# Performance work log

Measured on AMD Instinct MI355X. Metric: run time of the kernel, lower is better.

## Reference

```python
import jax, jax.numpy as jnp
import numpy as np

B, T, E, H = 2, 2048, 1024, 16
S = E // H
LN_EPS = 1e-5


def _layer_norm(x, w, b):
    # normalize over last axis (head dim s)
    mu = jnp.mean(x, axis=-1, keepdims=True)
    var = jnp.mean(jnp.square(x - mu), axis=-1, keepdims=True)
    return (x - mu) * jax.lax.rsqrt(var + LN_EPS) * w + b


def setup_inputs() -> dict:
    key = jax.random.key(0)
    ks = jax.random.split(key, 7)
    scale = 0.02
    return {
        "queries": jax.random.normal(ks[0], (B, T, E), dtype=jnp.float32),
        "keys": jax.random.normal(ks[1], (B, T, E), dtype=jnp.float32),
        "values": jax.random.normal(ks[2], (B, T, E), dtype=jnp.float32),
        "Wq": jax.random.normal(ks[3], (E, E), dtype=jnp.float32) * scale,
        "Wk": jax.random.normal(ks[4], (E, E), dtype=jnp.float32) * scale,
        "Wv": jax.random.normal(ks[5], (E, E), dtype=jnp.float32) * scale,
        "Wo": jax.random.normal(ks[6], (E, E), dtype=jnp.float32) * scale,
        "bo": jnp.zeros((E,), dtype=jnp.float32),
        "q_ln_w": jnp.ones((S,), dtype=jnp.float32),
        "q_ln_b": jnp.zeros((S,), dtype=jnp.float32),
        "k_ln_w": jnp.ones((S,), dtype=jnp.float32),
        "k_ln_b": jnp.zeros((S,), dtype=jnp.float32),
    }


def reference(queries, keys, values, Wq, Wk, Wv, Wo, bo, q_ln_w, q_ln_b, k_ln_w, k_ln_b):
    b, tq, e = queries.shape
    tk = keys.shape[1]
    h, s = H, S

    q = (queries @ Wq).reshape(b, tq, h, s)
    k = (keys @ Wk).reshape(b, tk, h, s)
    v = (values @ Wv).reshape(b, tk, h, s)

    # kqnorm: per-head LayerNorm over s
    q = _layer_norm(q, q_ln_w, q_ln_b)
    k = _layer_norm(k, k_ln_w, k_ln_b)

    # NOTE: original scales q and k each by emb**(-1/4) (NOT head_dim)
    inv4 = jnp.asarray(e, q.dtype) ** -0.25
    q = q * inv4
    k = k * inv4

    dot = jnp.einsum("bqhs,bkhs->bhqk", q, k)  # [b,h,tq,tk]

    # causal mask (mask_diagonal=False -> keep diagonal): mask j > i
    causal = jnp.tril(jnp.ones((tq, tk), dtype=bool))
    dot = jnp.where(causal, dot, jnp.asarray(-jnp.inf, dot.dtype))

    attn = jax.nn.softmax(dot, axis=-1)

    out = jnp.einsum("bhqk,bkhs->bqhs", attn, v).reshape(b, tq, e)
    return out @ Wo + bo
```

## Files before the change

### kernel.cpp

```cpp
#include <hip/hip_runtime.h>

#define Tdim 2048
#define Edim 1024
#define Hdim 16
#define Sdim 64
#define Mdim 4096
#define LN_EPS 1e-5f
#define QKSCALE 0.21233045007200477f

typedef __bf16 bf16x8 __attribute__((ext_vector_type(8)));
typedef float f32x4 __attribute__((ext_vector_type(4)));

__device__ __forceinline__ unsigned short f2bf(float f) {
  union { float f; unsigned int u; } c; c.f = f;
  unsigned int u = c.u;
  return (unsigned short)((u + 0x7FFFu + ((u >> 16) & 1u)) >> 16);
}

__device__ __forceinline__ float exp2fast(float x) {
  float r;
  asm("v_exp_f32 %0, %1" : "=v"(r) : "v"(x));
  return r;
}

__device__ __forceinline__ void gl_lds16(const void* g, void* l) {
  __builtin_amdgcn_global_load_lds(
      (const __attribute__((address_space(1))) void*)g,
      (__attribute__((address_space(3))) void*)l, 16, 0, 0);
}

__device__ __forceinline__ unsigned int pk2bf(unsigned int lo, unsigned int hi) {
  return __builtin_amdgcn_perm(hi, lo, 0x07060302u);
}

__global__ __launch_bounds__(256) void cvt_k(
    const float* __restrict__ X0, const float* __restrict__ X1, const float* __restrict__ X2,
    unsigned short* __restrict__ Y0, unsigned short* __restrict__ Y1,
    unsigned short* __restrict__ Y2) {
  const float* X = blockIdx.z == 0 ? X0 : blockIdx.z == 1 ? X1 : X2;
  unsigned short* Y = blockIdx.z == 0 ? Y0 : blockIdx.z == 1 ? Y1 : Y2;
  size_t i = ((size_t)blockIdx.x * 256 + threadIdx.x) * 8;
  uint4 a = *(const uint4*)&X[i];
  uint4 b = *(const uint4*)&X[i + 4];
  uint4 o;
  o.x = pk2bf(a.x, a.y);
  o.y = pk2bf(a.z, a.w);
  o.z = pk2bf(b.x, b.y);
  o.w = pk2bf(b.z, b.w);
  *(uint4*)&Y[i] = o;
}

__global__ __launch_bounds__(256) void wconv_k(
    const float* __restrict__ W0, const float* __restrict__ W1,
    const float* __restrict__ W2, const float* __restrict__ W3,
    unsigned short* __restrict__ O0, unsigned short* __restrict__ O1,
    unsigned short* __restrict__ O2, unsigned short* __restrict__ O3) {
  const float* W = blockIdx.z == 0 ? W0 : blockIdx.z == 1 ? W1 : blockIdx.z == 2 ? W2 : W3;
  unsigned short* O = blockIdx.z == 0 ? O0 : blockIdx.z == 1 ? O1 : blockIdx.z == 2 ? O2 : O3;
  __shared__ float tile[32][33];
  int n0 = blockIdx.x * 32, k0 = blockIdx.y * 32;
  int tx = threadIdx.x, ty = threadIdx.y;
  for (int yy = ty; yy < 32; yy += 8)
    tile[yy][tx] = W[(size_t)(k0 + yy) * Edim + n0 + tx];
  __syncthreads();
  for (int yy = ty; yy < 32; yy += 8)
    O[(size_t)(n0 + yy) * Edim + k0 + tx] = f2bf(tile[tx][yy]);
}

__global__ __launch_bounds__(256) void qkv_k(
    const unsigned short* __restrict__ Qa, const unsigned short* __restrict__ Ka,
    const unsigned short* __restrict__ Va,
    const unsigned short* __restrict__ Bq, const unsigned short* __restrict__ Bk,
    const unsigned short* __restrict__ Bv,
    const float* __restrict__ qlnw, const float* __restrict__ qlnb,
    const float* __restrict__ klnw, const float* __restrict__ klnb,
    unsigned short* __restrict__ Oq, unsigned short* __restrict__ Ok,
    unsigned short* __restrict__ Ov) {
  __shared__ unsigned short As[2][128 * 64];
  __shared__ unsigned short Bs[2][128 * 64];
  const int z = blockIdx.z;
  const unsigned short* A = z == 0 ? Qa : z == 1 ? Ka : Va;
  const unsigned short* Bt = z == 0 ? Bq : z == 1 ? Bk : Bv;
  const float* lnw = z == 0 ? qlnw : klnw;
  const float* lnb = z == 0 ? qlnb : klnb;
  unsigned short* obf = z == 0 ? Oq : z == 1 ? Ok : Ov;
  const bool doLN = z < 2;

  int tid = threadIdx.x, lane = tid & 63, w = tid >> 6;
  int wr = w >> 1, wc = w & 1;
  int lg = lane >> 4, l15 = lane & 15;
  int lr = lane >> 3, ls = lane & 7;
  int m0 = blockIdx.y * 128, n0 = blockIdx.x * 128;

  f32x4 acc[4][4];
#pragma unroll
  for (int i = 0; i < 4; ++i)
#pragma unroll
    for (int j = 0; j < 4; ++j) acc[i][j] = f32x4{0.f, 0.f, 0.f, 0.f};

  auto stage = [&](int buf, int ks) {
    int k0 = ks * 64;
#pragma unroll
    for (int q = 0; q < 4; ++q) {
      int c = w * 4 + q, r = c * 8 + lr;
      gl_lds16(&A[(size_t)(m0 + r) * Edim + k0 + ((ls ^ (r & 7)) * 8)], &As[buf][c * 512]);
    }
#pragma unroll
    for (int q = 0; q < 4; ++q) {
      int c = w * 4 + q, r = c * 8 + lr;
      gl_lds16(&Bt[(size_t)(n0 + r) * Edim + k0 + ((ls ^ (r & 7)) * 8)], &Bs[buf][c * 512]);
    }
  };

  stage(0, 0);
  for (int ks = 0; ks < 16; ++ks) {
    int cur = ks & 1;
    __syncthreads();
    if (ks + 1 < 16) stage(cur ^ 1, ks + 1);
    __builtin_amdgcn_s_setprio(1);
#pragma unroll
    for (int kx = 0; kx < 2; ++kx) {
      bf16x8 a[4], bb[4];
#pragma unroll
      for (int i = 0; i < 4; ++i) {
        int r = wr * 64 + i * 16 + l15;
        a[i] = *(const bf16x8*)&As[cur][r * 64 + (((kx * 4 + lg) ^ (r & 7)) * 8)];
      }
#pragma unroll
      for (int j = 0; j < 4; ++j) {
        int r = wc * 64 + j * 16 + l15;
        bb[j] = *(const bf16x8*)&Bs[cur][r * 64 + (((kx * 4 + lg) ^ (r & 7)) * 8)];
      }
#pragma unroll
      for (int i = 0; i < 4; ++i)
#pragma unroll
        for (int j = 0; j < 4; ++j)
          acc[i][j] = __builtin_amdgcn_mfma_f32_16x16x32_bf16(a[i], bb[j], acc[i][j], 0, 0, 0);
    }
    __builtin_amdgcn_s_setprio(0);
  }

  int mb = m0 + wr * 64;
  int h = (n0 >> 6) + wc;
#pragma unroll
  for (int i = 0; i < 4; ++i) {
#pragma unroll
    for (int r = 0; r < 4; ++r) {
      float xv[4];
#pragma unroll
      for (int j = 0; j < 4; ++j) xv[j] = acc[i][j][r];
      float outv[4];
      if (doLN) {
        float sum = xv[0] + xv[1] + xv[2] + xv[3];
        float sq = xv[0] * xv[0] + xv[1] * xv[1] + xv[2] * xv[2] + xv[3] * xv[3];
#pragma unroll
        for (int off = 1; off < 16; off <<= 1) {
          sum += __shfl_xor(sum, off);
          sq += __shfl_xor(sq, off);
        }
        float mean = sum * (1.f / 64.f);
        float var = sq * (1.f / 64.f) - mean * mean;
        float rstd = rsqrtf(var + LN_EPS);
#pragma unroll
        for (int j = 0; j < 4; ++j) {
          int s = j * 16 + l15;
          outv[j] = ((xv[j] - mean) * rstd * lnw[s] + lnb[s]) * QKSCALE;
        }
      } else {
#pragma unroll
        for (int j = 0; j < 4; ++j) outv[j] = xv[j];
      }
      int m = mb + i * 16 + (lg << 2) + r;
      int bb2 = m >> 11, tt = m & 2047;
      size_t base = ((size_t)(bb2 * Hdim + h) * Tdim + tt) * Sdim;
#pragma unroll
      for (int j = 0; j < 4; ++j) obf[base + j * 16 + l15] = f2bf(outv[j]);
    }
  }
}

__global__ __launch_bounds__(256) void gemmo_k(
    const unsigned short* __restrict__ A, const unsigned short* __restrict__ Bt,
    const float* __restrict__ bias, float* __restrict__ ofp) {
  __shared__ unsigned short As[2][128 * 64];
  __shared__ unsigned short Bs[2][64 * 64];
  int tid = threadIdx.x, lane = tid & 63, w = tid >> 6;
  int wr = w >> 1, wc = w & 1;
  int lg = lane >> 4, l15 = lane & 15;
  int lr = lane >> 3, ls = lane & 7;
  int m0 = blockIdx.y * 128, n0 = blockIdx.x * 64;

  f32x4 acc[4][2];
#pragma unroll
  for (int i = 0; i < 4; ++i)
#pragma unroll
    for (int j = 0; j < 2; ++j) acc[i][j] = f32x4{0.f, 0.f, 0.f, 0.f};

  auto stage = [&](int buf, int ks) {
    int k0 = ks * 64;
#pragma unroll
    for (int q = 0; q < 4; ++q) {
      int c = w * 4 + q, r = c * 8 + lr;
      gl_lds16(&A[(size_t)(m0 + r) * Edim + k0 + ((ls ^ (r & 7)) * 8)], &As[buf][c * 512]);
    }
#pragma unroll
    for (int q = 0; q < 2; ++q) {
      int c = w * 2 + q, r = c * 8 + lr;
      gl_lds16(&Bt[(size_t)(n0 + r) * Edim + k0 + ((ls ^ (r & 7)) * 8)], &Bs[buf][c * 512]);
    }
  };

  stage(0, 0);
  for (int ks = 0; ks < 16; ++ks) {
    int cur = ks & 1;
    __syncthreads();
    if (ks + 1 < 16) stage(cur ^ 1, ks + 1);
    __builtin_amdgcn_s_setprio(1);
#pragma unroll
    for (int kx = 0; kx < 2; ++kx) {
      bf16x8 a[4], bb[2];
#pragma unroll
      for (int i = 0; i < 4; ++i) {
        int r = wr * 64 + i * 16 + l15;
        a[i] = *(const bf16x8*)&As[cur][r * 64 + (((kx * 4 + lg) ^ (r & 7)) * 8)];
      }
#pragma unroll
      for (int j = 0; j < 2; ++j) {
        int r = wc * 32 + j * 16 + l15;
        bb[j] = *(const bf16x8*)&Bs[cur][r * 64 + (((kx * 4 + lg) ^ (r & 7)) * 8)];
      }
#pragma unroll
      for (int i = 0; i < 4; ++i)
#pragma unroll
        for (int j = 0; j < 2; ++j)
          acc[i][j] = __builtin_amdgcn_mfma_f32_16x16x32_bf16(a[i], bb[j], acc[i][j], 0, 0, 0);
    }
    __builtin_amdgcn_s_setprio(0);
  }

  int mb = m0 + wr * 64, nb = n0 + wc * 32;
#pragma unroll
  for (int i = 0; i < 4; ++i)
#pragma unroll
    for (int r = 0; r < 4; ++r) {
      int m = mb + i * 16 + (lg << 2) + r;
#pragma unroll
      for (int j = 0; j < 2; ++j) {
        int n = nb + j * 16 + l15;
        ofp[(size_t)m * Edim + n] = acc[i][j][r] + bias[n];
      }
    }
}

__global__ __launch_bounds__(256) void flash_k(
    const unsigned short* __restrict__ Qn, const unsigned short* __restrict__ Kn,
    const unsigned short* __restrict__ Vb, unsigned short* __restrict__ Ob) {
  __shared__ unsigned short Qs[64 * 64];
  __shared__ unsigned short Ks[2][64 * 64];
  __shared__ unsigned short Vt[2][64 * 64];
  __shared__ unsigned short Ps[4][16 * 64];

  int wid0 = blockIdx.y * gridDim.x + blockIdx.x;
  int wid = (wid0 & 7) * 64 + (wid0 >> 3);
  int x = wid & 15, bh = wid >> 4;

  int tid = threadIdx.x, lane = tid & 63, w = tid >> 6;
  int lg = lane >> 4, l15 = lane & 15;
  int lr = lane >> 3, ls = lane & 7;
  int vl = tid >> 4, vs0 = (tid & 15) * 4;
  const unsigned short* Kg = Kn + (size_t)bh * Tdim * Sdim;
  const unsigned short* Vg = Vb + (size_t)bh * Tdim * Sdim;
  int b = bh >> 4, h = bh & 15;

  uint2 vreg[4];
  auto ldV = [&](int t) {
    const unsigned short* p = Vg + (size_t)t * 64 * 64;
#pragma unroll
    for (int j = 0; j < 4; ++j) vreg[j] = *(const uint2*)&p[(j * 16 + vl) * 64 + vs0];
  };
  auto stV = [&](unsigned short* dst) {
#pragma unroll
    for (int st = 0; st < 4; ++st) {
      int s = vs0 + st;
      unsigned int e[4];
#pragma unroll
      for (int j = 0; j < 4; ++j) {
        unsigned int wrd = (st & 2) ? vreg[j].y : vreg[j].x;
        e[j] = (st & 1) ? (wrd >> 16) : (wrd & 0xffffu);
      }
      uint2 wv;
      wv.x = e[0] | (e[1] << 16);
      wv.y = e[2] | (e[3] << 16);
      *(uint2*)((char*)dst + s * 128 + (((vl >> 1) ^ (s & 7)) * 16) + (vl & 1) * 8) = wv;
    }
  };

  for (int ph = 0; ph < 2; ++ph) {
    int qseg = ph ? (31 - x) : x;
    const unsigned short* Qg = Qn + ((size_t)bh * Tdim + (size_t)qseg * 64) * Sdim;
    int nt = qseg + 1;

#pragma unroll
    for (int q = 0; q < 2; ++q) {
      int c = w * 2 + q, r = c * 8 + lr;
      gl_lds16(&Qg[(size_t)r * 64 + ((ls ^ (r & 7)) * 8)], &Qs[c * 512]);
      gl_lds16(&Kg[(size_t)r * 64 + ((ls ^ (r & 7)) * 8)], &Ks[0][c * 512]);
    }
    ldV(0);
    stV(&Vt[0][0]);

    f32x4 sf[4], o[4];
    float mrun[4], lrun[4];
#pragma unroll
    for (int r = 0; r < 4; ++r) {
      mrun[r] = -1e30f;
      lrun[r] = 0.f;
      o[r] = f32x4{0.f, 0.f, 0.f, 0.f};
    }
    __syncthreads();

    for (int t = 0; t < nt; ++t) {
      int cur = t & 1;
      if (t + 1 < nt) {
#pragma unroll
        for (int q = 0; q < 2; ++q) {
          int c = w * 2 + q, r = c * 8 + lr;
          gl_lds16(&Kg[((size_t)(t + 1) * 64 + r) * 64 + ((ls ^ (r & 7)) * 8)],
                   &Ks[cur ^ 1][c * 512]);
        }
        ldV(t + 1);
      }
#pragma unroll
      for (int j = 0; j < 4; ++j) sf[j] = f32x4{0.f, 0.f, 0.f, 0.f};
      __builtin_amdgcn_s_setprio(1);
#pragma unroll
      for (int kx = 0; kx < 2; ++kx) {
        int rq = w * 16 + l15;
        bf16x8 aq = *(const bf16x8*)&Qs[rq * 64 + (((kx * 4 + lg) ^ (rq & 7)) * 8)];
#pragma unroll
        for (int j = 0; j < 4; ++j) {
          int rk = j * 16 + l15;
          bf16x8 bk = *(const bf16x8*)&Ks[cur][rk * 64 + (((kx * 4 + lg) ^ (rk & 7)) * 8)];
          sf[j] = __builtin_amdgcn_mfma_f32_16x16x32_bf16(aq, bk, sf[j], 0, 0, 0);
        }
      }
      __builtin_amdgcn_s_setprio(0);
      if (t == qseg) {
#pragma unroll
        for (int j = 0; j < 4; ++j)
#pragma unroll
          for (int rr = 0; rr < 4; ++rr)
            if (j * 16 + l15 > w * 16 + (lg << 2) + rr) sf[j][rr] = -1e30f;
      }
      float mx[4];
#pragma unroll
      for (int rr = 0; rr < 4; ++rr) {
        float m0v = fmaxf(fmaxf(sf[0][rr], sf[1][rr]), fmaxf(sf[2][rr], sf[3][rr]));
#pragma unroll
        for (int off = 1; off < 16; off <<= 1) m0v = fmaxf(m0v, __shfl_xor(m0v, off));
        mx[rr] = m0v;
      }
      int fastok = (mx[0] <= mrun[0] + 8.f) && (mx[1] <= mrun[1] + 8.f) &&
                   (mx[2] <= mrun[2] + 8.f) && (mx[3] <= mrun[3] + 8.f);
      if (!__all(fastok)) {
#pragma unroll
        for (int rr = 0; rr < 4; ++rr) {
          float mnew = fmaxf(mrun[rr], mx[rr]);
          float alpha = exp2fast(mrun[rr] - mnew);
          mrun[rr] = mnew;
          lrun[rr] *= alpha;
#pragma unroll
          for (int js = 0; js < 4; ++js) o[js][rr] *= alpha;
        }
      }
#pragma unroll
      for (int rr = 0; rr < 4; ++rr) {
        float p0 = exp2fast(sf[0][rr] - mrun[rr]);
        float p1 = exp2fast(sf[1][rr] - mrun[rr]);
        float p2 = exp2fast(sf[2][rr] - mrun[rr]);
        float p3 = exp2fast(sf[3][rr] - mrun[rr]);
        lrun[rr] += (p0 + p1) + (p2 + p3);
        union { float f; unsigned int u; } c0{p0}, c1{p1}, c2{p2}, c3{p3};
        uint2 wv;
        wv.x = pk2bf(c0.u, c1.u);
        wv.y = pk2bf(c2.u, c3.u);
        int qr = (lg << 2) + rr;
        *(uint2*)((char*)&Ps[w][0] + qr * 128 + (((l15 >> 1) ^ (qr & 7)) * 16) +
                  (l15 & 1) * 8) = wv;
      }
      __builtin_amdgcn_s_setprio(1);
#pragma unroll
      for (int kx = 0; kx < 2; ++kx) {
        bf16x8 ap = *(const bf16x8*)((char*)&Ps[w][0] + l15 * 128 +
                                     (((kx * 4 + lg) ^ (l15 & 7)) * 16));
#pragma unroll
        for (int js = 0; js < 4; ++js) {
          int rv = js * 16 + l15;
          bf16x8 bv = *(const bf16x8*)((char*)&Vt[cur][0] + rv * 128 +
                                       (((kx * 4 + lg) ^ (rv & 7)) * 16));
          o[js] = __builtin_amdgcn_mfma_f32_16x16x32_bf16(ap, bv, o[js], 0, 0, 0);
        }
      }
      __builtin_amdgcn_s_setprio(0);
      if (t + 1 < nt) stV(&Vt[cur ^ 1][0]);
      __syncthreads();
    }

#pragma unroll
    for (int rr = 0; rr < 4; ++rr) {
      float l = lrun[rr];
#pragma unroll
      for (int off = 1; off < 16; off <<= 1) l += __shfl_xor(l, off);
      float inv = 1.f / l;
      int tg = qseg * 64 + w * 16 + (lg << 2) + rr;
      size_t base = ((size_t)b * Tdim + tg) * Edim + h * 64;
#pragma unroll
      for (int js = 0; js < 4; ++js) Ob[base + js * 16 + l15] = f2bf(o[js][rr] * inv);
    }
  }
}

extern "C" void kernel_launch(void* const* d_in, const int* in_sizes, int n_in,
                              void* d_out, int out_size, void* d_ws, size_t ws_size,
                              hipStream_t stream) {
  const float* queries = (const float*)d_in[0];
  const float* keys    = (const float*)d_in[1];
  const float* values  = (const float*)d_in[2];
  const float* Wq = (const float*)d_in[3];
  const float* Wk = (const float*)d_in[4];
  const float* Wv = (const float*)d_in[5];
  const float* Wo = (const float*)d_in[6];
  const float* bo = (const float*)d_in[7];
  const float* qlnw = (const float*)d_in[8];
  const float* qlnb = (const float*)d_in[9];
  const float* klnw = (const float*)d_in[10];
  const float* klnb = (const float*)d_in[11];
  float* out = (float*)d_out;

  unsigned short* Wtq = (unsigned short*)d_ws;
  unsigned short* Wtk = Wtq + 1024 * 1024;
  unsigned short* Wtv = Wtk + 1024 * 1024;
  unsigned short* Wto = Wtv + 1024 * 1024;
  unsigned short* Qn  = Wto + 1024 * 1024;
  unsigned short* Kn  = Qn + (size_t)Mdim * Edim;
  unsigned short* Vb  = Kn + (size_t)Mdim * Edim;
  unsigned short* Qa  = Vb + (size_t)Mdim * Edim;
  unsigned short* Ka  = Qa + (size_t)Mdim * Edim;
  unsigned short* Va  = Ka + (size_t)Mdim * Edim;
  unsigned short* Ob  = Qa;

  cvt_k<<<dim3(2048, 1, 3), 256, 0, stream>>>(queries, keys, values, Qa, Ka, Va);
  wconv_k<<<dim3(32, 32, 4), dim3(32, 8), 0, stream>>>(Wq, Wk, Wv, Wo, Wtq, Wtk, Wtv, Wto);
  qkv_k<<<dim3(8, 32, 3), 256, 0, stream>>>(Qa, Ka, Va, Wtq, Wtk, Wtv,
                                            qlnw, qlnb, klnw, klnb, Qn, Kn, Vb);
  flash_k<<<dim3(16, 32), 256, 0, stream>>>(Qn, Kn, Vb, Ob);
  gemmo_k<<<dim3(16, 32), 256, 0, stream>>>(Ob, Wto, bo, out);
}
```

Baseline: 247.2 us.

## Pre-transpose V in projection, pipeline QK ahead of softmax, remap blocks

The QKV projection now writes V transposed as [b,h,s,t] by swapping operand roles for z==2, so the flash kernel can load V tiles straight into LDS with async global-to-LDS copies. This replaces the register load and in-LDS transpose. The flash kernel triple-buffers K and computes the next tile's QK^T before the current tile's softmax and PV, to overlap MFMA with exp work. It also keeps a single running max per wave instead of per row, and truncates P to bf16 instead of rounding. Both GEMMs use 1D grids with an XCD-aware block remap to improve L2 locality. The shared per-wave max and the truncation may cost some accuracy, and the transposed V stores are strided.

After: 275.5 us. +11.4%, slower.

```diff
diff --git a/kernel.cpp b/kernel.cpp
--- a/kernel.cpp
+++ b/kernel.cpp
@@ -78,19 +78,20 @@
     unsigned short* __restrict__ Ov) {
   __shared__ unsigned short As[2][128 * 64];
   __shared__ unsigned short Bs[2][128 * 64];
-  const int z = blockIdx.z;
+  int f = blockIdx.x;
+  int L = (f & 7) * 96 + (f >> 3);
+  int bx = L & 7, by = (L >> 3) & 31, z = L >> 8;
   const unsigned short* A = z == 0 ? Qa : z == 1 ? Ka : Va;
   const unsigned short* Bt = z == 0 ? Bq : z == 1 ? Bk : Bv;
   const float* lnw = z == 0 ? qlnw : klnw;
   const float* lnb = z == 0 ? qlnb : klnb;
   unsigned short* obf = z == 0 ? Oq : z == 1 ? Ok : Ov;
-  const bool doLN = z < 2;
 
   int tid = threadIdx.x, lane = tid & 63, w = tid >> 6;
   int wr = w >> 1, wc = w & 1;
   int lg = lane >> 4, l15 = lane & 15;
   int lr = lane >> 3, ls = lane & 7;
-  int m0 = blockIdx.y * 128, n0 = blockIdx.x * 128;
+  int m0 = by * 128, n0 = bx * 128;
 
   f32x4 acc[4][4];
 #pragma unroll
@@ -108,6 +109,118 @@
 #pragma unroll
     for (int q = 0; q < 4; ++q) {
       int c = w * 4 + q, r = c * 8 + lr;
+      gl_lds16(&Bt[(size_t)(n0 + r) * Edim + k0 + ((ls ^ (r & 7)) * 8)], &Bs[buf][c * 512]);
+    }
+  };
+
+  stage(0, 0);
+  for (int ks = 0; ks < 16; ++ks) {
+    int cur = ks & 1;
+    __syncthreads();
+    if (ks + 1 < 16) stage(cur ^ 1, ks + 1);
+    const unsigned short* pA = (z == 2) ? &Bs[cur][0] : &As[cur][0];
+    const unsigned short* pB = (z == 2) ? &As[cur][0] : &Bs[cur][0];
+    __builtin_amdgcn_s_setprio(1);
+#pragma unroll
+    for (int kx = 0; kx < 2; ++kx) {
+      bf16x8 a[4], bb[4];
+#pragma unroll
+      for (int i = 0; i < 4; ++i) {
+        int r = wr * 64 + i * 16 + l15;
+        a[i] = *(const bf16x8*)&pA[r * 64 + (((kx * 4 + lg) ^ (r & 7)) * 8)];
+      }
+#pragma unroll
+      for (int j = 0; j < 4; ++j) {
+        int r = wc * 64 + j * 16 + l15;
+        bb[j] = *(const bf16x8*)&pB[r * 64 + (((kx * 4 + lg) ^ (r & 7)) * 8)];
+      }
+#pragma unroll
+      for (int i = 0; i < 4; ++i)
+#pragma unroll
+        for (int j = 0; j < 4; ++j)
+          acc[i][j] = __builtin_amdgcn_mfma_f32_16x16x32_bf16(a[i], bb[j], acc[i][j], 0, 0, 0);
+    }
+    __builtin_amdgcn_s_setprio(0);
+  }
+
+  if (z < 2) {
+    int mb = m0 + wr * 64;
+    int h = (n0 >> 6) + wc;
+#pragma unroll
+    for (int i = 0; i < 4; ++i) {
+#pragma unroll
+      for (int r = 0; r < 4; ++r) {
+        float xv[4];
+#pragma unroll
+        for (int j = 0; j < 4; ++j) xv[j] = acc[i][j][r];
+        float sum = xv[0] + xv[1] + xv[2] + xv[3];
+        float sq = xv[0] * xv[0] + xv[1] * xv[1] + xv[2] * xv[2] + xv[3] * xv[3];
+#pragma unroll
+        for (int off = 1; off < 16; off <<= 1) {
+          sum += __shfl_xor(sum, off);
+          sq += __shfl_xor(sq, off);
+        }
+        float mean = sum * (1.f / 64.f);
+        float var = sq * (1.f / 64.f) - mean * mean;
+        float rstd = rsqrtf(var + LN_EPS);
+        int m = mb + i * 16 + (lg << 2) + r;
+        int bb2 = m >> 11, tt = m & 2047;
+        size_t base = ((size_t)(bb2 * Hdim + h) * Tdim + tt) * Sdim;
+#pragma unroll
+        for (int j = 0; j < 4; ++j) {
+          int s = j * 16 + l15;
+          float ov = ((xv[j] - mean) * rstd * lnw[s] + lnb[s]) * QKSCALE;
+          obf[base + s] = f2bf(ov);
+        }
+      }
+    }
+  } else {
+#pragma unroll
+    for (int i = 0; i < 4; ++i)
+#pragma unroll
+      for (int r = 0; r < 4; ++r) {
+        int hc = n0 + wr * 64 + i * 16 + (lg << 2) + r;
+        int h = hc >> 6, s = hc & 63;
+#pragma unroll
+        for (int j = 0; j < 4; ++j) {
+          int tk = m0 + wc * 64 + j * 16 + l15;
+          int bb2 = tk >> 11, tt = tk & 2047;
+          obf[(((size_t)(bb2 * Hdim + h) * Sdim + s)) * Tdim + tt] = f2bf(acc[i][j][r]);
+        }
+      }
+  }
+}
+
+__global__ __launch_bounds__(256) void gemmo_k(
+    const unsigned short* __restrict__ A, const unsigned short* __restrict__ Bt,
+    const float* __restrict__ bias, float* __restrict__ ofp) {
+  __shared__ unsigned short As[2][128 * 64];
+  __shared__ unsigned short Bs[2][64 * 64];
+  int f = blockIdx.x;
+  int L = (f & 7) * 64 + (f >> 3);
+  int bx = L & 15, by = L >> 4;
+  int tid = threadIdx.x, lane = tid & 63, w = tid >> 6;
+  int wr = w >> 1, wc = w & 1;
+  int lg = lane >> 4, l15 = lane & 15;
+  int lr = lane >> 3, ls = lane & 7;
+  int m0 = by * 128, n0 = bx * 64;
+
+  f32x4 acc[4][2];
+#pragma unroll
+  for (int i = 0; i < 4; ++i)
+#pragma unroll
+    for (int j = 0; j < 2; ++j) acc[i][j] = f32x4{0.f, 0.f, 0.f, 0.f};
+
+  auto stage = [&](int buf, int ks) {
+    int k0 = ks * 64;
+#pragma unroll
+    for (int q = 0; q < 4; ++q) {
+      int c = w * 4 + q, r = c * 8 + lr;
+      gl_lds16(&A[(size_t)(m0 + r) * Edim + k0 + ((ls ^ (r & 7)) * 8)], &As[buf][c * 512]);
+    }
+#pragma unroll
+    for (int q = 0; q < 2; ++q) {
+      int c = w * 2 + q, r = c * 8 + lr;
       gl_lds16(&Bt[(size_t)(n0 + r) * Edim + k0 + ((ls ^ (r & 7)) * 8)], &Bs[buf][c * 512]);
     }
   };
@@ -120,111 +233,13 @@
     __builtin_amdgcn_s_setprio(1);
 #pragma unroll
     for (int kx = 0; kx < 2; ++kx) {
-      bf16x8 a[4], bb[4];
+      bf16x8 a[4], bb[2];
 #pragma unroll
       for (int i = 0; i < 4; ++i) {
         int r = wr * 64 + i * 16 + l15;
         a[i] = *(const bf16x8*)&As[cur][r * 64 + (((kx * 4 + lg) ^ (r & 7)) * 8)];
       }
 #pragma unroll
-      for (int j = 0; j < 4; ++j) {
-        int r = wc * 64 + j * 16 + l15;
-        bb[j] = *(const bf16x8*)&Bs[cur][r * 64 + (((kx * 4 + lg) ^ (r & 7)) * 8)];
-      }
-#pragma unroll
-      for (int i = 0; i < 4; ++i)
-#pragma unroll
-        for (int j = 0; j < 4; ++j)
-          acc[i][j] = __builtin_amdgcn_mfma_f32_16x16x32_bf16(a[i], bb[j], acc[i][j], 0, 0, 0);
-    }
-    __builtin_amdgcn_s_setprio(0);
-  }
-
-  int mb = m0 + wr * 64;
-  int h = (n0 >> 6) + wc;
-#pragma unroll
-  for (int i = 0; i < 4; ++i) {
-#pragma unroll
-    for (int r = 0; r < 4; ++r) {
-      float xv[4];
-#pragma unroll
-      for (int j = 0; j < 4; ++j) xv[j] = acc[i][j][r];
-      float outv[4];
-      if (doLN) {
-        float sum = xv[0] + xv[1] + xv[2] + xv[3];
-        float sq = xv[0] * xv[0] + xv[1] * xv[1] + xv[2] * xv[2] + xv[3] * xv[3];
-#pragma unroll
-        for (int off = 1; off < 16; off <<= 1) {
-          sum += __shfl_xor(sum, off);
-          sq += __shfl_xor(sq, off);
-        }
-        float mean = sum * (1.f / 64.f);
-        float var = sq * (1.f / 64.f) - mean * mean;
-        float rstd = rsqrtf(var + LN_EPS);
-#pragma unroll
-        for (int j = 0; j < 4; ++j) {
-          int s = j * 16 + l15;
-          outv[j] = ((xv[j] - mean) * rstd * lnw[s] + lnb[s]) * QKSCALE;
-        }
-      } else {
-#pragma unroll
-        for (int j = 0; j < 4; ++j) outv[j] = xv[j];
-      }
-      int m = mb + i * 16 + (lg << 2) + r;
-      int bb2 = m >> 11, tt = m & 2047;
-      size_t base = ((size_t)(bb2 * Hdim + h) * Tdim + tt) * Sdim;
-#pragma unroll
-      for (int j = 0; j < 4; ++j) obf[base + j * 16 + l15] = f2bf(outv[j]);
-    }
-  }
-}
-
-__global__ __launch_bounds__(256) void gemmo_k(
-    const unsigned short* __restrict__ A, const unsigned short* __restrict__ Bt,
-    const float* __restrict__ bias, float* __restrict__ ofp) {
-  __shared__ unsigned short As[2][128 * 64];
-  __shared__ unsigned short Bs[2][64 * 64];
-  int tid = threadIdx.x, lane = tid & 63, w = tid >> 6;
-  int wr = w >> 1, wc = w & 1;
-  int lg = lane >> 4, l15 = lane & 15;
-  int lr = lane >> 3, ls = lane & 7;
-  int m0 = blockIdx.y * 128, n0 = blockIdx.x * 64;
-
-  f32x4 acc[4][2];
-#pragma unroll
-  for (int i = 0; i < 4; ++i)
-#pragma unroll
-    for (int j = 0; j < 2; ++j) acc[i][j] = f32x4{0.f, 0.f, 0.f, 0.f};
-
-  auto stage = [&](int buf, int ks) {
-    int k0 = ks * 64;
-#pragma unroll
-    for (int q = 0; q < 4; ++q) {
-      int c = w * 4 + q, r = c * 8 + lr;
-      gl_lds16(&A[(size_t)(m0 + r) * Edim + k0 + ((ls ^ (r & 7)) * 8)], &As[buf][c * 512]);
-    }
-#pragma unroll
-    for (int q = 0; q < 2; ++q) {
-      int c = w * 2 + q, r = c * 8 + lr;
-      gl_lds16(&Bt[(size_t)(n0 + r) * Edim + k0 + ((ls ^ (r & 7)) * 8)], &Bs[buf][c * 512]);
-    }
-  };
-
-  stage(0, 0);
-  for (int ks = 0; ks < 16; ++ks) {
-    int cur = ks & 1;
-    __syncthreads();
-    if (ks + 1 < 16) stage(cur ^ 1, ks + 1);
-    __builtin_amdgcn_s_setprio(1);
-#pragma unroll
-    for (int kx = 0; kx < 2; ++kx) {
-      bf16x8 a[4], bb[2];
-#pragma unroll
-      for (int i = 0; i < 4; ++i) {
-        int r = wr * 64 + i * 16 + l15;
-        a[i] = *(const bf16x8*)&As[cur][r * 64 + (((kx * 4 + lg) ^ (r & 7)) * 8)];
-      }
-#pragma unroll
       for (int j = 0; j < 2; ++j) {
         int r = wc * 32 + j * 16 + l15;
         bb[j] = *(const bf16x8*)&Bs[cur][r * 64 + (((kx * 4 + lg) ^ (r & 7)) * 8)];
@@ -255,10 +270,10 @@
 __global__ __launch_bounds__(256) void flash_k(
     const unsigned short* __restrict__ Qn, const unsigned short* __restrict__ Kn,
     const unsigned short* __restrict__ Vb, unsigned short* __restrict__ Ob) {
-  __shared__ unsigned short Qs[64 * 64];
-  __shared__ unsigned short Ks[2][64 * 64];
-  __shared__ unsigned short Vt[2][64 * 64];
-  __shared__ unsigned short Ps[4][16 * 64];
+  __shared__ unsigned short Qs[4096];
+  __shared__ unsigned short Ks[3][4096];
+  __shared__ unsigned short Vt[2][4096];
+  __shared__ unsigned short Ps[4][1024];
 
   int wid0 = blockIdx.y * gridDim.x + blockIdx.x;
   int wid = (wid0 & 7) * 64 + (wid0 >> 3);
@@ -267,142 +282,135 @@
   int tid = threadIdx.x, lane = tid & 63, w = tid >> 6;
   int lg = lane >> 4, l15 = lane & 15;
   int lr = lane >> 3, ls = lane & 7;
-  int vl = tid >> 4, vs0 = (tid & 15) * 4;
   const unsigned short* Kg = Kn + (size_t)bh * Tdim * Sdim;
-  const unsigned short* Vg = Vb + (size_t)bh * Tdim * Sdim;
+  const unsigned short* Vg = Vb + (size_t)bh * Sdim * Tdim;
   int b = bh >> 4, h = bh & 15;
 
-  uint2 vreg[4];
-  auto ldV = [&](int t) {
-    const unsigned short* p = Vg + (size_t)t * 64 * 64;
-#pragma unroll
-    for (int j = 0; j < 4; ++j) vreg[j] = *(const uint2*)&p[(j * 16 + vl) * 64 + vs0];
+  auto stageK = [&](int tt, int kb) {
+    const unsigned short* src = Kg + (size_t)tt * 64 * 64;
+#pragma unroll
+    for (int q = 0; q < 2; ++q) {
+      int c = w * 2 + q, r = c * 8 + lr;
+      gl_lds16(&src[r * 64 + ((ls ^ (r & 7)) * 8)], &Ks[kb][c * 512]);
+    }
   };
-  auto stV = [&](unsigned short* dst) {
-#pragma unroll
-    for (int st = 0; st < 4; ++st) {
-      int s = vs0 + st;
-      unsigned int e[4];
-#pragma unroll
-      for (int j = 0; j < 4; ++j) {
-        unsigned int wrd = (st & 2) ? vreg[j].y : vreg[j].x;
-        e[j] = (st & 1) ? (wrd >> 16) : (wrd & 0xffffu);
-      }
-      uint2 wv;
-      wv.x = e[0] | (e[1] << 16);
-      wv.y = e[2] | (e[3] << 16);
-      *(uint2*)((char*)dst + s * 128 + (((vl >> 1) ^ (s & 7)) * 16) + (vl & 1) * 8) = wv;
+  auto stageV = [&](int tt, int vb) {
+    const unsigned short* src = Vg + tt * 64;
+#pragma unroll
+    for (int q = 0; q < 2; ++q) {
+      int c = w * 2 + q, r = c * 8 + lr;
+      gl_lds16(&src[(size_t)r * Tdim + ((ls ^ (r & 7)) * 8)], &Vt[vb][c * 512]);
     }
   };
 
   for (int ph = 0; ph < 2; ++ph) {
     int qseg = ph ? (31 - x) : x;
+    int nt = qseg + 1;
     const unsigned short* Qg = Qn + ((size_t)bh * Tdim + (size_t)qseg * 64) * Sdim;
-    int nt = qseg + 1;
 
 #pragma unroll
     for (int q = 0; q < 2; ++q) {
       int c = w * 2 + q, r = c * 8 + lr;
-      gl_lds16(&Qg[(size_t)r * 64 + ((ls ^ (r & 7)) * 8)], &Qs[c * 512]);
-      gl_lds16(&Kg[(size_t)r * 64 + ((ls ^ (r & 7)) * 8)], &Ks[0][c * 512]);
-    }
-    ldV(0);
-    stV(&Vt[0][0]);
-
-    f32x4 sf[4], o[4];
-    float mrun[4], lrun[4];
-#pragma unroll
-    for (int r = 0; r < 4; ++r) {
-      mrun[r] = -1e30f;
-      lrun[r] = 0.f;
-      o[r] = f32x4{0.f, 0.f, 0.f, 0.f};
-    }
+      gl_lds16(&Qg[r * 64 + ((ls ^ (r & 7)) * 8)], &Qs[c * 512]);
+    }
+    stageK(0, 0);
+    if (nt > 1) stageK(1, 1);
+    stageV(0, 0);
+
+    float mrun = -1e30f;
+    float lrun[4] = {0.f, 0.f, 0.f, 0.f};
+    f32x4 o[4];
+#pragma unroll
+    for (int js = 0; js < 4; ++js) o[js] = f32x4{0.f, 0.f, 0.f, 0.f};
+
     __syncthreads();
 
-    for (int t = 0; t < nt; ++t) {
-      int cur = t & 1;
-      if (t + 1 < nt) {
-#pragma unroll
-        for (int q = 0; q < 2; ++q) {
-          int c = w * 2 + q, r = c * 8 + lr;
-          gl_lds16(&Kg[((size_t)(t + 1) * 64 + r) * 64 + ((ls ^ (r & 7)) * 8)],
-                   &Ks[cur ^ 1][c * 512]);
-        }
-        ldV(t + 1);
-      }
-#pragma unroll
-      for (int j = 0; j < 4; ++j) sf[j] = f32x4{0.f, 0.f, 0.f, 0.f};
+    bf16x8 aq[2];
+    {
+      int rq = w * 16 + l15;
+      aq[0] = *(const bf16x8*)&Qs[rq * 64 + ((lg ^ (rq & 7)) * 8)];
+      aq[1] = *(const bf16x8*)&Qs[rq * 64 + (((4 + lg) ^ (rq & 7)) * 8)];
+    }
+
+    auto QK = [&](f32x4(&dst)[4], int tt) {
+      const unsigned short* Kc = &Ks[tt % 3][0];
+#pragma unroll
+      for (int j = 0; j < 4; ++j) dst[j] = f32x4{0.f, 0.f, 0.f, 0.f};
       __builtin_amdgcn_s_setprio(1);
 #pragma unroll
       for (int kx = 0; kx < 2; ++kx) {
-        int rq = w * 16 + l15;
-        bf16x8 aq = *(const bf16x8*)&Qs[rq * 64 + (((kx * 4 + lg) ^ (rq & 7)) * 8)];
 #pragma unroll
         for (int j = 0; j < 4; ++j) {
           int rk = j * 16 + l15;
-          bf16x8 bk = *(const bf16x8*)&Ks[cur][rk * 64 + (((kx * 4 + lg) ^ (rk & 7)) * 8)];
-          sf[j] = __builtin_amdgcn_mfma_f32_16x16x32_bf16(aq, bk, sf[j], 0, 0, 0);
+          bf16x8 bk = *(const bf16x8*)&Kc[rk * 64 + (((kx * 4 + lg) ^ (rk & 7)) * 8)];
+          dst[j] = __builtin_amdgcn_mfma_f32_16x16x32_bf16(aq[kx], bk, dst[j], 0, 0, 0);
         }
       }
       __builtin_amdgcn_s_setprio(0);
-      if (t == qseg) {
+    };
+
+    auto SMPV = [&](f32x4(&cur)[4], int t) {
+      if (t == nt - 1) {
 #pragma unroll
         for (int j = 0; j < 4; ++j)
 #pragma unroll
           for (int rr = 0; rr < 4; ++rr)
-            if (j * 16 + l15 > w * 16 + (lg << 2) + rr) sf[j][rr] = -1e30f;
-      }
-      float mx[4];
-#pragma unroll
-      for (int rr = 0; rr < 4; ++rr) {
-        float m0v = fmaxf(fmaxf(sf[0][rr], sf[1][rr]), fmaxf(sf[2][rr], sf[3][rr]));
-#pragma unroll
-        for (int off = 1; off < 16; off <<= 1) m0v = fmaxf(m0v, __shfl_xor(m0v, off));
-        mx[rr] = m0v;
-      }
-      int fastok = (mx[0] <= mrun[0] + 8.f) && (mx[1] <= mrun[1] + 8.f) &&
-                   (mx[2] <= mrun[2] + 8.f) && (mx[3] <= mrun[3] + 8.f);
-      if (!__all(fastok)) {
+            if (j * 16 + l15 > w * 16 + (lg << 2) + rr) cur[j][rr] = -1e30f;
+      }
+      float mx = -3e38f;
+#pragma unroll
+      for (int j = 0; j < 4; ++j)
+#pragma unroll
+        for (int rr = 0; rr < 4; ++rr) mx = fmaxf(mx, cur[j][rr]);
+#pragma unroll
+      for (int off = 1; off < 16; off <<= 1) mx = fmaxf(mx, __shfl_xor(mx, off));
+      if (__any(mx > mrun + 8.f)) {
+        float mnew = fmaxf(mrun, mx);
+        float alpha = exp2fast(mrun - mnew);
+        mrun = mnew;
+#pragma unroll
+        for (int rr = 0; rr < 4; ++rr) lrun[rr] *= alpha;
+#pragma unroll
+        for (int js = 0; js < 4; ++js) o[js] *= alpha;
+      }
+      unsigned short* Pw = &Ps[w][0];
+#pragma unroll
+      for (int j = 0; j < 4; ++j) {
+        int og = 2 * j + (l15 >> 3);
 #pragma unroll
         for (int rr = 0; rr < 4; ++rr) {
-          float mnew = fmaxf(mrun[rr], mx[rr]);
-          float alpha = exp2fast(mrun[rr] - mnew);
-          mrun[rr] = mnew;
-          lrun[rr] *= alpha;
-#pragma unroll
-          for (int js = 0; js < 4; ++js) o[js][rr] *= alpha;
-        }
-      }
-#pragma unroll
-      for (int rr = 0; rr < 4; ++rr) {
-        float p0 = exp2fast(sf[0][rr] - mrun[rr]);
-        float p1 = exp2fast(sf[1][rr] - mrun[rr]);
-        float p2 = exp2fast(sf[2][rr] - mrun[rr]);
-        float p3 = exp2fast(sf[3][rr] - mrun[rr]);
-        lrun[rr] += (p0 + p1) + (p2 + p3);
-        union { float f; unsigned int u; } c0{p0}, c1{p1}, c2{p2}, c3{p3};
-        uint2 wv;
-        wv.x = pk2bf(c0.u, c1.u);
-        wv.y = pk2bf(c2.u, c3.u);
-        int qr = (lg << 2) + rr;
-        *(uint2*)((char*)&Ps[w][0] + qr * 128 + (((l15 >> 1) ^ (qr & 7)) * 16) +
-                  (l15 & 1) * 8) = wv;
-      }
+          float p = exp2fast(cur[j][rr] - mrun);
+          lrun[rr] += p;
+          union { float f; unsigned int u; } cu;
+          cu.f = p;
+          int qr = (lg << 2) + rr;
+          Pw[qr * 64 + ((og ^ (qr & 7)) * 8) + (l15 & 7)] = (unsigned short)(cu.u >> 16);
+        }
+      }
+      const unsigned short* Vc = &Vt[t & 1][0];
       __builtin_amdgcn_s_setprio(1);
 #pragma unroll
       for (int kx = 0; kx < 2; ++kx) {
-        bf16x8 ap = *(const bf16x8*)((char*)&Ps[w][0] + l15 * 128 +
-                                     (((kx * 4 + lg) ^ (l15 & 7)) * 16));
+        bf16x8 ap = *(const bf16x8*)&Pw[l15 * 64 + (((kx * 4 + lg) ^ (l15 & 7)) * 8)];
 #pragma unroll
         for (int js = 0; js < 4; ++js) {
           int rv = js * 16 + l15;
-          bf16x8 bv = *(const bf16x8*)((char*)&Vt[cur][0] + rv * 128 +
-                                       (((kx * 4 + lg) ^ (rv & 7)) * 16));
+          bf16x8 bv = *(const bf16x8*)&Vc[rv * 64 + (((kx * 4 + lg) ^ (rv & 7)) * 8)];
           o[js] = __builtin_amdgcn_mfma_f32_16x16x32_bf16(ap, bv, o[js], 0, 0, 0);
         }
       }
       __builtin_amdgcn_s_setprio(0);
-      if (t + 1 < nt) stV(&Vt[cur ^ 1][0]);
+    };
+
+    f32x4 sA[4], sB[4];
+    QK(sA, 0);
+    for (int t = 0; t < nt; ++t) {
+      if (t + 2 < nt) stageK(t + 2, (t + 2) % 3);
+      if (t + 1 < nt) stageV(t + 1, (t + 1) & 1);
+      if (t + 1 < nt) {
+        if (t & 1) QK(sA, t + 1); else QK(sB, t + 1);
+      }
+      if (t & 1) SMPV(sB, t); else SMPV(sA, t);
       __syncthreads();
     }
 
@@ -451,8 +459,8 @@
 
   cvt_k<<<dim3(2048, 1, 3), 256, 0, stream>>>(queries, keys, values, Qa, Ka, Va);
   wconv_k<<<dim3(32, 32, 4), dim3(32, 8), 0, stream>>>(Wq, Wk, Wv, Wo, Wtq, Wtk, Wtv, Wto);
-  qkv_k<<<dim3(8, 32, 3), 256, 0, stream>>>(Qa, Ka, Va, Wtq, Wtk, Wtv,
-                                            qlnw, qlnb, klnw, klnb, Qn, Kn, Vb);
+  qkv_k<<<768, 256, 0, stream>>>(Qa, Ka, Va, Wtq, Wtk, Wtv,
+                                 qlnw, qlnb, klnw, klnb, Qn, Kn, Vb);
   flash_k<<<dim3(16, 32), 256, 0, stream>>>(Qn, Kn, Vb, Ob);
-  gemmo_k<<<dim3(16, 32), 256, 0, stream>>>(Ob, Wto, bo, out);
-}
+  gemmo_k<<<512, 256, 0, stream>>>(Ob, Wto, bo, out);
+}
```
